# Performance work log

Measured on AMD Instinct MI355X. Metric: run time of the kernel, lower is better.

The kernel has to match this reference:

```python
import jax, jax.numpy as jnp
import numpy as np

B, T, Z, S, H = 32, 128, 100, 6, 64
F1, F2 = 512, 128


def setup_inputs() -> dict:
    key = jax.random.key(0)
    ks = jax.random.split(key, 11)
    g = lambda k, shape, sc: (jax.random.normal(k, shape, dtype=jnp.float32) * sc)
    return {
        "x": jax.random.normal(ks[0], (B, T, Z, S), dtype=jnp.float32),
        "W_ih": g(ks[1], (3 * H, S), 0.125),   # GRU input weights [r|z|n]
        "W_hh": g(ks[2], (3 * H, H), 0.125),   # GRU hidden weights [r|z|n]
        "b_ih": g(ks[3], (3 * H,), 0.125),
        "b_hh": g(ks[4], (3 * H,), 0.125),
        "w1": g(ks[5], (F1, H), 0.1),
        "b1": g(ks[6], (F1,), 0.1),
        "w2": g(ks[7], (F2, F1), 0.04),
        "b2": g(ks[8], (F2,), 0.04),
        "w3": g(ks[9], (1, F2), 0.09),
        "b3": g(ks[10], (1,), 0.09),
    }


def reference(x, W_ih, W_hh, b_ih, b_hh, w1, b1, w2, b2, w3, b3):
    b, t, z, s = x.shape
    h_dim = W_hh.shape[1]
    # Fuse the per-zone python loop into the batch dim, zone-major so the
    # final reshape matches torch.stack(a).view(-1, t, nzones).
    xm = jnp.transpose(x, (2, 0, 1, 3)).reshape(z * b, t, s)  # (ZB, T, S)
    # Precompute input projections for all timesteps (one big GEMM).
    gi_all = jnp.einsum('nts,gs->ntg', xm, W_ih) + b_ih        # (ZB, T, 3H)

    def step(h, gi):
        gh = h @ W_hh.T + b_hh
        r = jax.nn.sigmoid(gi[:, :h_dim] + gh[:, :h_dim])
        zg = jax.nn.sigmoid(gi[:, h_dim:2 * h_dim] + gh[:, h_dim:2 * h_dim])
        n = jnp.tanh(gi[:, 2 * h_dim:] + r * gh[:, 2 * h_dim:])
        h_new = (1.0 - zg) * n + zg * h
        return h_new, h_new

    h0 = jnp.zeros((z * b, h_dim), x.dtype)
    _, sx = jax.lax.scan(step, h0, jnp.swapaxes(gi_all, 0, 1))  # (T, ZB, H)
    sx = jnp.swapaxes(sx, 0, 1)                                  # (ZB, T, H)

    a1 = jax.nn.relu(sx @ w1.T + b1)
    a2 = jax.nn.relu(a1 @ w2.T + b2)
    a3 = a2 @ w3.T + b3                                          # (ZB, T, 1)
    return a3.reshape(-1, t, z)                                  # (B, T, Z)
```

## Files before the change

### kernel.cpp

```cpp
#include <hip/hip_runtime.h>
#include <stdint.h>

#define Tdim 128
#define Zdim 100
#define Sdim 6
#define Hdim 64
#define ZB   3200
#define F1   512
#define F2   128
#define Mrows (ZB * Tdim)

typedef _Float16 f16x8 __attribute__((ext_vector_type(8)));
typedef _Float16 f16x4 __attribute__((ext_vector_type(4)));
typedef float f32x4 __attribute__((ext_vector_type(4)));
typedef uint32_t u32x4 __attribute__((ext_vector_type(4)));

__device__ __forceinline__ float fast_rcp(float x) {
  return __builtin_amdgcn_rcpf(x);
}

__global__ __launch_bounds__(256) void prep_kernel(
    const float* __restrict__ W_ih, const float* __restrict__ W_hh,
    const float* __restrict__ w1, const float* __restrict__ w2,
    _Float16* __restrict__ Wf, _Float16* __restrict__ w1p,
    _Float16* __restrict__ w2p) {
  int i = blockIdx.x * 256 + threadIdx.x;
  if (i < 192 * 96) {
    int g = i / 96, k = i - g * 96;
    float v = (k < 64) ? W_hh[g * 64 + k] : ((k < 70) ? W_ih[g * 6 + (k - 64)] : 0.f);
    Wf[i] = (_Float16)v;
  }
  int j = i - 192 * 96;
  if (j >= 0 && j < 32768) {
    int kt = j >> 11, ntl = (j >> 10) & 1, kf = (j >> 9) & 1;
    int lane = (j >> 3) & 63, e = j & 7;
    int q = lane >> 4, c = lane & 15;
    int row = kt * 32 + ntl * 16 + c;
    int h = kf * 32 + q * 8 + e;
    w1p[j] = (_Float16)w1[row * 64 + h];
  }
  int l = j - 32768;
  if (l >= 0 && l < 65536) {
    int kt = l >> 12, nt = (l >> 9) & 7;
    int lane = (l >> 3) & 63, e = l & 7;
    int q = lane >> 4, c = lane & 15;
    int row = nt * 16 + c;
    int k = kt * 32 + q * 8 + e;
    w2p[l] = (_Float16)w2[row * 512 + k];
  }
}

__global__ __launch_bounds__(512, 1) void gru_kernel(
    const float* __restrict__ x, const _Float16* __restrict__ Wf,
    const float* __restrict__ b_ih, const float* __restrict__ b_hh,
    _Float16* __restrict__ sx) {
  __shared__ __align__(16) _Float16 hist[16][32][72];
  __shared__ __align__(16) _Float16 xs[Tdim][32][8];
  const int tid = threadIdx.x;
  const int lane = tid & 63;
  const int w8 = tid >> 6;
  const int s = w8 >> 2;
  const int w = w8 & 3;
  const int c = lane & 15;
  const int q = lane >> 4;
  const int s16c = s * 16 + c;

  for (int i = 0; i < 8; i++) {
    int idx = i * 512 + tid;
    int t = idx >> 5, row = idx & 31;
    int nr = blockIdx.x * 32 + row;
    const float* p = x + (size_t)(nr & 31) * (Tdim * Zdim * Sdim)
                       + (size_t)t * (Zdim * Sdim) + (size_t)(nr >> 5) * Sdim;
    f16x8 v;
    v[0] = (_Float16)p[0]; v[1] = (_Float16)p[1]; v[2] = (_Float16)p[2];
    v[3] = (_Float16)p[3]; v[4] = (_Float16)p[4]; v[5] = (_Float16)p[5];
    v[6] = (_Float16)0.f;  v[7] = (_Float16)0.f;
    *(f16x8*)&xs[t][row][0] = v;
  }

  const int gr0 = w * 16;
  const int gz0 = 64 + w * 16;
  const int gn0 = 128 + w * 16;

  f16x8 Ar[3], Az[3], Anh[2], Ani;
#pragma unroll
  for (int kf = 0; kf < 3; kf++) {
    Ar[kf] = *(const f16x8*)(Wf + (size_t)(gr0 + c) * 96 + kf * 32 + q * 8);
    Az[kf] = *(const f16x8*)(Wf + (size_t)(gz0 + c) * 96 + kf * 32 + q * 8);
  }
  Anh[0] = *(const f16x8*)(Wf + (size_t)(gn0 + c) * 96 + q * 8);
  Anh[1] = *(const f16x8*)(Wf + (size_t)(gn0 + c) * 96 + 32 + q * 8);
  Ani    = *(const f16x8*)(Wf + (size_t)(gn0 + c) * 96 + 64 + q * 8);

  f32x4 Cr, Cz, Cnh, Cni;
  {
    f32x4 bir = *(const f32x4*)(b_ih + gr0 + q * 4);
    f32x4 bhr = *(const f32x4*)(b_hh + gr0 + q * 4);
    f32x4 biz = *(const f32x4*)(b_ih + gz0 + q * 4);
    f32x4 bhz = *(const f32x4*)(b_hh + gz0 + q * 4);
#pragma unroll
    for (int r = 0; r < 4; r++) { Cr[r] = bir[r] + bhr[r]; Cz[r] = biz[r] + bhz[r]; }
    Cnh = *(const f32x4*)(b_hh + gn0 + q * 4);
    Cni = *(const f32x4*)(b_ih + gn0 + q * 4);
  }

  const uint32_t xmask = (q == 0) ? 0xffffffffu : 0u;

  __syncthreads();

  f16x8 Bh0 = {0, 0, 0, 0, 0, 0, 0, 0};
  f16x8 Bh1 = {0, 0, 0, 0, 0, 0, 0, 0};
  f32x4 hprev = {0.f, 0.f, 0.f, 0.f};

  f32x4 Dr_s, Dz_s, Dni_s;
  {
    u32x4 xv = *(const u32x4*)&xs[0][s16c][0];
    xv[0] &= xmask; xv[1] &= xmask; xv[2] &= xmask; xv[3] &= xmask;
    f16x8 Bx = *(f16x8*)&xv;
    Dni_s = __builtin_amdgcn_mfma_f32_16x16x32_f16(Ani, Bx, Cni, 0, 0, 0);
    Dr_s  = __builtin_amdgcn_mfma_f32_16x16x32_f16(Ar[2], Bx, Cr, 0, 0, 0);
    Dz_s  = __builtin_amdgcn_mfma_f32_16x16x32_f16(Az[2], Bx, Cz, 0, 0, 0);
  }

#pragma unroll 1
  for (int tch = 0; tch < 8; tch++) {
#pragma unroll 1
    for (int tc = 0; tc < 16; tc++) {
      const int t = tch * 16 + tc;
      f32x4 Dnh = __builtin_amdgcn_mfma_f32_16x16x32_f16(Anh[0], Bh0, Cnh, 0, 0, 0);
      f32x4 Dr  = __builtin_amdgcn_mfma_f32_16x16x32_f16(Ar[0], Bh0, Dr_s, 0, 0, 0);
      f32x4 Dz  = __builtin_amdgcn_mfma_f32_16x16x32_f16(Az[0], Bh0, Dz_s, 0, 0, 0);
      Dnh = __builtin_amdgcn_mfma_f32_16x16x32_f16(Anh[1], Bh1, Dnh, 0, 0, 0);
      Dr  = __builtin_amdgcn_mfma_f32_16x16x32_f16(Ar[1], Bh1, Dr, 0, 0, 0);
      Dz  = __builtin_amdgcn_mfma_f32_16x16x32_f16(Az[1], Bh1, Dz, 0, 0, 0);

      f16x4 pk;
#pragma unroll
      for (int r = 0; r < 4; r++) {
        float er = __expf(-Dr[r]);
        float rr = fast_rcp(1.f + er);
        float ez = __expf(-Dz[r]);
        float zg = fast_rcp(1.f + ez);
        float na = Dni_s[r] + rr * Dnh[r];
        float en = __expf(2.f * na);
        float nn = 1.f - 2.f * fast_rcp(en + 1.f);
        float hnew = nn + zg * (hprev[r] - nn);
        hprev[r] = hnew;
        pk[r] = (_Float16)hnew;
      }
      *(f16x4*)&hist[tc][s16c][w * 16 + q * 4] = pk;

      if (t + 1 < Tdim) {
        u32x4 xv = *(const u32x4*)&xs[t + 1][s16c][0];
        xv[0] &= xmask; xv[1] &= xmask; xv[2] &= xmask; xv[3] &= xmask;
        f16x8 Bx = *(f16x8*)&xv;
        Dni_s = __builtin_amdgcn_mfma_f32_16x16x32_f16(Ani, Bx, Cni, 0, 0, 0);
        Dr_s  = __builtin_amdgcn_mfma_f32_16x16x32_f16(Ar[2], Bx, Cr, 0, 0, 0);
        Dz_s  = __builtin_amdgcn_mfma_f32_16x16x32_f16(Az[2], Bx, Cz, 0, 0, 0);
      }
      __syncthreads();
      Bh0 = *(const f16x8*)&hist[tc][s16c][q * 8];
      Bh1 = *(const f16x8*)&hist[tc][s16c][32 + q * 8];
    }
    {
      const int t0 = tch * 16;
#pragma unroll
      for (int rr2 = 0; rr2 < 4; rr2++) {
        const int row = w8 * 4 + rr2;
        const int nrow = blockIdx.x * 32 + row;
        _Float16* dst = sx + (size_t)nrow * Tdim * Hdim + (size_t)t0 * Hdim;
#pragma unroll
        for (int it = 0; it < 2; it++) {
          int idx = it * 64 + lane;
          int tcc = idx >> 3, hd8 = idx & 7;
          f16x8 vv = *(const f16x8*)&hist[tcc][row][hd8 * 8];
          *(f16x8*)(dst + tcc * 64 + hd8 * 8) = vv;
        }
      }
      __syncthreads();
    }
  }
}

__global__ __launch_bounds__(256, 2) void mlp_kernel(
    const _Float16* __restrict__ sx, const _Float16* __restrict__ w1p,
    const _Float16* __restrict__ w2p, const float* __restrict__ b1,
    const float* __restrict__ b2, const float* __restrict__ w3,
    const float* __restrict__ b3, float* __restrict__ out) {
  __shared__ __align__(16) _Float16 w1s[32768];
  __shared__ __align__(16) _Float16 rep[4][4][512];
  const int tid = threadIdx.x;
  const int lane = tid & 63;
  const int wave = tid >> 6;
  const int c = lane & 15;
  const int q = lane >> 4;
  const size_t m0 = ((size_t)blockIdx.x * 4 + wave) * 64;

  {
    const u32x4* src = (const u32x4*)w1p;
    u32x4* dst = (u32x4*)w1s;
#pragma unroll
    for (int i = 0; i < 16; i++)
      dst[i * 256 + tid] = src[i * 256 + tid];
  }

  f16x8 Bs[4][2];
#pragma unroll
  for (int g = 0; g < 4; g++)
#pragma unroll
    for (int kk = 0; kk < 2; kk++)
      Bs[g][kk] = *(const f16x8*)(sx + (m0 + g * 16 + c) * Hdim + kk * 32 + q * 8);

  f32x4 acc2[4][8];
#pragma unroll
  for (int g = 0; g < 4; g++)
#pragma unroll
    for (int nt = 0; nt < 8; nt++) acc2[g][nt] = (f32x4){0.f, 0.f, 0.f, 0.f};

  __syncthreads();

  {
#pragma unroll
    for (int ntl = 0; ntl < 2; ntl++) {
      f16x8 A0 = *(const f16x8*)&w1s[ntl * 1024 + lane * 8];
      f16x8 A1 = *(const f16x8*)&w1s[ntl * 1024 + 512 + lane * 8];
      f32x4 bb = *(const f32x4*)(b1 + ntl * 16 + q * 4);
      const int roff = ((2 * ntl + (q >> 1)) * 16 + c) * 8 + (q & 1) * 4;
#pragma unroll
      for (int g = 0; g < 4; g++) {
        f32x4 cc = __builtin_amdgcn_mfma_f32_16x16x32_f16(A0, Bs[g][0], bb, 0, 0, 0);
        cc = __builtin_amdgcn_mfma_f32_16x16x32_f16(A1, Bs[g][1], cc, 0, 0, 0);
        f16x4 pk;
#pragma unroll
        for (int r = 0; r < 4; r++)
          pk[r] = (_Float16)(cc[r] > 0.f ? cc[r] : 0.f);
        *(f16x4*)&rep[wave][g][roff] = pk;
      }
    }
  }

#pragma unroll 1
  for (int kt = 0; kt < 16; kt++) {
    const int ktn = kt + 1;
    const bool more = (ktn < 16);
    f16x8 A2[8];
#pragma unroll
    for (int nt = 0; nt < 8; nt++)
      A2[nt] = *(const f16x8*)(w2p + (size_t)kt * 4096 + nt * 512 + lane * 8);
    f16x8 W0[2], W1[2];
    f32x4 bb[2];
    {
      const int kts = more ? ktn : kt;
#pragma unroll
      for (int ntl = 0; ntl < 2; ntl++) {
        W0[ntl] = *(const f16x8*)&w1s[kts * 2048 + ntl * 1024 + lane * 8];
        W1[ntl] = *(const f16x8*)&w1s[kts * 2048 + ntl * 1024 + 512 + lane * 8];
        bb[ntl] = *(const f32x4*)(b1 + kts * 32 + ntl * 16 + q * 4);
      }
    }
    f16x8 Ba[4];
#pragma unroll
    for (int g = 0; g < 4; g++)
      Ba[g] = *(const f16x8*)&rep[wave][g][lane * 8];

    if (more) {
#pragma unroll
      for (int ntl = 0; ntl < 2; ntl++) {
        const int roff = ((2 * ntl + (q >> 1)) * 16 + c) * 8 + (q & 1) * 4;
#pragma unroll
        for (int g = 0; g < 4; g++) {
          f32x4 cc = __builtin_amdgcn_mfma_f32_16x16x32_f16(W0[ntl], Bs[g][0], bb[ntl], 0, 0, 0);
          cc = __builtin_amdgcn_mfma_f32_16x16x32_f16(W1[ntl], Bs[g][1], cc, 0, 0, 0);
          f16x4 pk;
#pragma unroll
          for (int r = 0; r < 4; r++)
            pk[r] = (_Float16)(cc[r] > 0.f ? cc[r] : 0.f);
          *(f16x4*)&rep[wave][g][roff] = pk;
        }
      }
    }

#pragma unroll
    for (int nt = 0; nt < 8; nt++)
#pragma unroll
      for (int g = 0; g < 4; g++)
        acc2[g][nt] = __builtin_amdgcn_mfma_f32_16x16x32_f16(A2[nt], Ba[g], acc2[g][nt], 0, 0, 0);
  }

  float part[4] = {0.f, 0.f, 0.f, 0.f};
#pragma unroll
  for (int nt = 0; nt < 8; nt++) {
    f32x4 bb = *(const f32x4*)(b2 + nt * 16 + q * 4);
    f32x4 ww = *(const f32x4*)(w3 + nt * 16 + q * 4);
#pragma unroll
    for (int g = 0; g < 4; g++) {
#pragma unroll
      for (int r = 0; r < 4; r++) {
        float v = acc2[g][nt][r] + bb[r];
        v = v > 0.f ? v : 0.f;
        part[g] = fmaf(v, ww[r], part[g]);
      }
    }
  }
#pragma unroll
  for (int g = 0; g < 4; g++) {
    part[g] += __shfl_xor(part[g], 16, 64);
    part[g] += __shfl_xor(part[g], 32, 64);
  }
  float pv = (q == 0) ? part[0] : (q == 1) ? part[1] : (q == 2) ? part[2] : part[3];
  out[m0 + q * 16 + c] = pv + b3[0];
}

extern "C" void kernel_launch(void* const* d_in, const int* in_sizes, int n_in,
                              void* d_out, int out_size, void* d_ws, size_t ws_size,
                              hipStream_t stream) {
  const float* x    = (const float*)d_in[0];
  const float* W_ih = (const float*)d_in[1];
  const float* W_hh = (const float*)d_in[2];
  const float* b_ih = (const float*)d_in[3];
  const float* b_hh = (const float*)d_in[4];
  const float* w1   = (const float*)d_in[5];
  const float* b1   = (const float*)d_in[6];
  const float* w2   = (const float*)d_in[7];
  const float* b2   = (const float*)d_in[8];
  const float* w3   = (const float*)d_in[9];
  const float* b3   = (const float*)d_in[10];
  float* out = (float*)d_out;

  char* ws = (char*)d_ws;
  _Float16* sxf = (_Float16*)ws;
  _Float16* Wf  = (_Float16*)(ws + 52428800);
  _Float16* w1p = (_Float16*)(ws + 52428800 + 36864);
  _Float16* w2p = (_Float16*)(ws + 52428800 + 36864 + 65536);

  hipLaunchKernelGGL(prep_kernel, dim3(456), dim3(256), 0, stream,
                     W_ih, W_hh, w1, w2, Wf, w1p, w2p);
  hipLaunchKernelGGL(gru_kernel, dim3(ZB / 32), dim3(512), 0, stream,
                     x, Wf, b_ih, b_hh, sxf);
  hipLaunchKernelGGL(mlp_kernel, dim3(Mrows / 256), dim3(256), 0, stream,
                     sxf, w1p, w2p, b1, b2, w3, b3, out);
}
```

Baseline: 239.8 us.

## Fuse GRU and MLP into one producer-consumer kernel with chunk flags

```diff
diff --git a/kernel.cpp b/kernel.cpp
--- a/kernel.cpp
+++ b/kernel.cpp
@@ -9,6 +9,8 @@
 #define F1   512
 #define F2   128
 #define Mrows (ZB * Tdim)
+#define NGRU 100
+#define NMLP 800
 
 typedef _Float16 f16x8 __attribute__((ext_vector_type(8)));
 typedef _Float16 f16x4 __attribute__((ext_vector_type(4)));
@@ -23,8 +25,9 @@
     const float* __restrict__ W_ih, const float* __restrict__ W_hh,
     const float* __restrict__ w1, const float* __restrict__ w2,
     _Float16* __restrict__ Wf, _Float16* __restrict__ w1p,
-    _Float16* __restrict__ w2p) {
+    _Float16* __restrict__ w2p, unsigned int* __restrict__ sync) {
   int i = blockIdx.x * 256 + threadIdx.x;
+  if (i < 801) sync[i] = 0u;
   if (i < 192 * 96) {
     int g = i / 96, k = i - g * 96;
     float v = (k < 64) ? W_hh[g * 64 + k] : ((k < 70) ? W_ih[g * 6 + (k - 64)] : 0.f);
@@ -50,265 +53,288 @@
   }
 }
 
-__global__ __launch_bounds__(512, 1) void gru_kernel(
+__global__ __launch_bounds__(512, 2) void fused_kernel(
     const float* __restrict__ x, const _Float16* __restrict__ Wf,
     const float* __restrict__ b_ih, const float* __restrict__ b_hh,
-    _Float16* __restrict__ sx) {
-  __shared__ __align__(16) _Float16 hist[16][32][72];
-  __shared__ __align__(16) _Float16 xs[Tdim][32][8];
+    _Float16* __restrict__ sx, const _Float16* __restrict__ w1p,
+    const _Float16* __restrict__ w2p, const float* __restrict__ b1,
+    const float* __restrict__ b2, const float* __restrict__ w3,
+    const float* __restrict__ b3, float* __restrict__ out,
+    unsigned int* __restrict__ flags, unsigned int* __restrict__ ticket) {
+  union SmemU {
+    struct { _Float16 hist[16][32][72]; _Float16 xs[Tdim][32][8]; } g;
+    struct { _Float16 w1s[32768]; _Float16 rep[8][4][512]; } m;
+  };
+  __shared__ __align__(16) SmemU smem;
+  __shared__ int s_tk;
   const int tid = threadIdx.x;
+  if (tid == 0) s_tk = (int)atomicAdd(ticket, 1u);
+  __syncthreads();
+  const int tk = s_tk;
+
   const int lane = tid & 63;
   const int w8 = tid >> 6;
-  const int s = w8 >> 2;
-  const int w = w8 & 3;
   const int c = lane & 15;
   const int q = lane >> 4;
-  const int s16c = s * 16 + c;
-
-  for (int i = 0; i < 8; i++) {
-    int idx = i * 512 + tid;
-    int t = idx >> 5, row = idx & 31;
-    int nr = blockIdx.x * 32 + row;
-    const float* p = x + (size_t)(nr & 31) * (Tdim * Zdim * Sdim)
-                       + (size_t)t * (Zdim * Sdim) + (size_t)(nr >> 5) * Sdim;
-    f16x8 v;
-    v[0] = (_Float16)p[0]; v[1] = (_Float16)p[1]; v[2] = (_Float16)p[2];
-    v[3] = (_Float16)p[3]; v[4] = (_Float16)p[4]; v[5] = (_Float16)p[5];
-    v[6] = (_Float16)0.f;  v[7] = (_Float16)0.f;
-    *(f16x8*)&xs[t][row][0] = v;
-  }
-
-  const int gr0 = w * 16;
-  const int gz0 = 64 + w * 16;
-  const int gn0 = 128 + w * 16;
-
-  f16x8 Ar[3], Az[3], Anh[2], Ani;
-#pragma unroll
-  for (int kf = 0; kf < 3; kf++) {
-    Ar[kf] = *(const f16x8*)(Wf + (size_t)(gr0 + c) * 96 + kf * 32 + q * 8);
-    Az[kf] = *(const f16x8*)(Wf + (size_t)(gz0 + c) * 96 + kf * 32 + q * 8);
-  }
-  Anh[0] = *(const f16x8*)(Wf + (size_t)(gn0 + c) * 96 + q * 8);
-  Anh[1] = *(const f16x8*)(Wf + (size_t)(gn0 + c) * 96 + 32 + q * 8);
-  Ani    = *(const f16x8*)(Wf + (size_t)(gn0 + c) * 96 + 64 + q * 8);
-
-  f32x4 Cr, Cz, Cnh, Cni;
-  {
-    f32x4 bir = *(const f32x4*)(b_ih + gr0 + q * 4);
-    f32x4 bhr = *(const f32x4*)(b_hh + gr0 + q * 4);
-    f32x4 biz = *(const f32x4*)(b_ih + gz0 + q * 4);
-    f32x4 bhz = *(const f32x4*)(b_hh + gz0 + q * 4);
-#pragma unroll
-    for (int r = 0; r < 4; r++) { Cr[r] = bir[r] + bhr[r]; Cz[r] = biz[r] + bhz[r]; }
-    Cnh = *(const f32x4*)(b_hh + gn0 + q * 4);
-    Cni = *(const f32x4*)(b_ih + gn0 + q * 4);
-  }
-
-  const uint32_t xmask = (q == 0) ? 0xffffffffu : 0u;
-
-  __syncthreads();
-
-  f16x8 Bh0 = {0, 0, 0, 0, 0, 0, 0, 0};
-  f16x8 Bh1 = {0, 0, 0, 0, 0, 0, 0, 0};
-  f32x4 hprev = {0.f, 0.f, 0.f, 0.f};
-
-  f32x4 Dr_s, Dz_s, Dni_s;
-  {
-    u32x4 xv = *(const u32x4*)&xs[0][s16c][0];
-    xv[0] &= xmask; xv[1] &= xmask; xv[2] &= xmask; xv[3] &= xmask;
-    f16x8 Bx = *(f16x8*)&xv;
-    Dni_s = __builtin_amdgcn_mfma_f32_16x16x32_f16(Ani, Bx, Cni, 0, 0, 0);
-    Dr_s  = __builtin_amdgcn_mfma_f32_16x16x32_f16(Ar[2], Bx, Cr, 0, 0, 0);
-    Dz_s  = __builtin_amdgcn_mfma_f32_16x16x32_f16(Az[2], Bx, Cz, 0, 0, 0);
-  }
+
+  if (tk < NGRU) {
+    const int gb = tk;
+    auto& hist = smem.g.hist;
+    auto& xs = smem.g.xs;
+    const int s = w8 >> 2;
+    const int w = w8 & 3;
+    const int s16c = s * 16 + c;
+
+    for (int i = 0; i < 8; i++) {
+      int idx = i * 512 + tid;
+      int t = idx >> 5, row = idx & 31;
+      int nr = gb * 32 + row;
+      const float* p = x + (size_t)(nr & 31) * (Tdim * Zdim * Sdim)
+                         + (size_t)t * (Zdim * Sdim) + (size_t)(nr >> 5) * Sdim;
+      f16x8 v;
+      v[0] = (_Float16)p[0]; v[1] = (_Float16)p[1]; v[2] = (_Float16)p[2];
+      v[3] = (_Float16)p[3]; v[4] = (_Float16)p[4]; v[5] = (_Float16)p[5];
+      v[6] = (_Float16)0.f;  v[7] = (_Float16)0.f;
+      *(f16x8*)&xs[t][row][0] = v;
+    }
+
+    const int gr0 = w * 16;
+    const int gz0 = 64 + w * 16;
+    const int gn0 = 128 + w * 16;
+
+    f16x8 Ar[3], Az[3], Anh[2], Ani;
+#pragma unroll
+    for (int kf = 0; kf < 3; kf++) {
+      Ar[kf] = *(const f16x8*)(Wf + (size_t)(gr0 + c) * 96 + kf * 32 + q * 8);
+      Az[kf] = *(const f16x8*)(Wf + (size_t)(gz0 + c) * 96 + kf * 32 + q * 8);
+    }
+    Anh[0] = *(const f16x8*)(Wf + (size_t)(gn0 + c) * 96 + q * 8);
+    Anh[1] = *(const f16x8*)(Wf + (size_t)(gn0 + c) * 96 + 32 + q * 8);
+    Ani    = *(const f16x8*)(Wf + (size_t)(gn0 + c) * 96 + 64 + q * 8);
+
+    f32x4 Cr, Cz, Cnh, Cni;
+    {
+      f32x4 bir = *(const f32x4*)(b_ih + gr0 + q * 4);
+      f32x4 bhr = *(const f32x4*)(b_hh + gr0 + q * 4);
+      f32x4 biz = *(const f32x4*)(b_ih + gz0 + q * 4);
+      f32x4 bhz = *(const f32x4*)(b_hh + gz0 + q * 4);
+#pragma unroll
+      for (int r = 0; r < 4; r++) { Cr[r] = bir[r] + bhr[r]; Cz[r] = biz[r] + bhz[r]; }
+      Cnh = *(const f32x4*)(b_hh + gn0 + q * 4);
+      Cni = *(const f32x4*)(b_ih + gn0 + q * 4);
+    }
+
+    const uint32_t xmask = (q == 0) ? 0xffffffffu : 0u;
+
+    __syncthreads();
+
+    f16x8 Bh0 = {0, 0, 0, 0, 0, 0, 0, 0};
+    f16x8 Bh1 = {0, 0, 0, 0, 0, 0, 0, 0};
+    f32x4 hprev = {0.f, 0.f, 0.f, 0.f};
+
+    f32x4 Dr_s, Dz_s, Dni_s;
+    {
+      u32x4 xv = *(const u32x4*)&xs[0][s16c][0];
+      xv[0] &= xmask; xv[1] &= xmask; xv[2] &= xmask; xv[3] &= xmask;
+      f16x8 Bx = *(f16x8*)&xv;
+      Dni_s = __builtin_amdgcn_mfma_f32_16x16x32_f16(Ani, Bx, Cni, 0, 0, 0);
+      Dr_s  = __builtin_amdgcn_mfma_f32_16x16x32_f16(Ar[2], Bx, Cr, 0, 0, 0);
+      Dz_s  = __builtin_amdgcn_mfma_f32_16x16x32_f16(Az[2], Bx, Cz, 0, 0, 0);
+    }
 
 #pragma unroll 1
-  for (int tch = 0; tch < 8; tch++) {
+    for (int tch = 0; tch < 8; tch++) {
 #pragma unroll 1
-    for (int tc = 0; tc < 16; tc++) {
-      const int t = tch * 16 + tc;
-      f32x4 Dnh = __builtin_amdgcn_mfma_f32_16x16x32_f16(Anh[0], Bh0, Cnh, 0, 0, 0);
-      f32x4 Dr  = __builtin_amdgcn_mfma_f32_16x16x32_f16(Ar[0], Bh0, Dr_s, 0, 0, 0);
-      f32x4 Dz  = __builtin_amdgcn_mfma_f32_16x16x32_f16(Az[0], Bh0, Dz_s, 0, 0, 0);
-      Dnh = __builtin_amdgcn_mfma_f32_16x16x32_f16(Anh[1], Bh1, Dnh, 0, 0, 0);
-      Dr  = __builtin_amdgcn_mfma_f32_16x16x32_f16(Ar[1], Bh1, Dr, 0, 0, 0);
-      Dz  = __builtin_amdgcn_mfma_f32_16x16x32_f16(Az[1], Bh1, Dz, 0, 0, 0);
-
-      f16x4 pk;
-#pragma unroll
-      for (int r = 0; r < 4; r++) {
-        float er = __expf(-Dr[r]);
-        float rr = fast_rcp(1.f + er);
-        float ez = __expf(-Dz[r]);
-        float zg = fast_rcp(1.f + ez);
-        float na = Dni_s[r] + rr * Dnh[r];
-        float en = __expf(2.f * na);
-        float nn = 1.f - 2.f * fast_rcp(en + 1.f);
-        float hnew = nn + zg * (hprev[r] - nn);
-        hprev[r] = hnew;
-        pk[r] = (_Float16)hnew;
-      }
-      *(f16x4*)&hist[tc][s16c][w * 16 + q * 4] = pk;
-
-      if (t + 1 < Tdim) {
-        u32x4 xv = *(const u32x4*)&xs[t + 1][s16c][0];
-        xv[0] &= xmask; xv[1] &= xmask; xv[2] &= xmask; xv[3] &= xmask;
-        f16x8 Bx = *(f16x8*)&xv;
-        Dni_s = __builtin_amdgcn_mfma_f32_16x16x32_f16(Ani, Bx, Cni, 0, 0, 0);
-        Dr_s  = __builtin_amdgcn_mfma_f32_16x16x32_f16(Ar[2], Bx, Cr, 0, 0, 0);
-        Dz_s  = __builtin_amdgcn_mfma_f32_16x16x32_f16(Az[2], Bx, Cz, 0, 0, 0);
-      }
-      __syncthreads();
-      Bh0 = *(const f16x8*)&hist[tc][s16c][q * 8];
-      Bh1 = *(const f16x8*)&hist[tc][s16c][32 + q * 8];
-    }
+      for (int tc = 0; tc < 16; tc++) {
+        const int t = tch * 16 + tc;
+        f32x4 Dnh = __builtin_amdgcn_mfma_f32_16x16x32_f16(Anh[0], Bh0, Cnh, 0, 0, 0);
+        f32x4 Dr  = __builtin_amdgcn_mfma_f32_16x16x32_f16(Ar[0], Bh0, Dr_s, 0, 0, 0);
+        f32x4 Dz  = __builtin_amdgcn_mfma_f32_16x16x32_f16(Az[0], Bh0, Dz_s, 0, 0, 0);
+        Dnh = __builtin_amdgcn_mfma_f32_16x16x32_f16(Anh[1], Bh1, Dnh, 0, 0, 0);
+        Dr  = __builtin_amdgcn_mfma_f32_16x16x32_f16(Ar[1], Bh1, Dr, 0, 0, 0);
+        Dz  = __builtin_amdgcn_mfma_f32_16x16x32_f16(Az[1], Bh1, Dz, 0, 0, 0);
+
+        f16x4 pk;
+#pragma unroll
+        for (int r = 0; r < 4; r++) {
+          float er = __expf(-Dr[r]);
+          float rr = fast_rcp(1.f + er);
+          float ez = __expf(-Dz[r]);
+          float zg = fast_rcp(1.f + ez);
+          float na = Dni_s[r] + rr * Dnh[r];
+          float en = __expf(2.f * na);
+          float nn = 1.f - 2.f * fast_rcp(en + 1.f);
+          float hnew = nn + zg * (hprev[r] - nn);
+          hprev[r] = hnew;
+          pk[r] = (_Float16)hnew;
+        }
+        *(f16x4*)&hist[tc][s16c][w * 16 + q * 4] = pk;
+
+        if (t + 1 < Tdim) {
+          u32x4 xv = *(const u32x4*)&xs[t + 1][s16c][0];
+          xv[0] &= xmask; xv[1] &= xmask; xv[2] &= xmask; xv[3] &= xmask;
+          f16x8 Bx = *(f16x8*)&xv;
+          Dni_s = __builtin_amdgcn_mfma_f32_16x16x32_f16(Ani, Bx, Cni, 0, 0, 0);
+          Dr_s  = __builtin_amdgcn_mfma_f32_16x16x32_f16(Ar[2], Bx, Cr, 0, 0, 0);
+          Dz_s  = __builtin_amdgcn_mfma_f32_16x16x32_f16(Az[2], Bx, Cz, 0, 0, 0);
+        }
+        __syncthreads();
+        Bh0 = *(const f16x8*)&hist[tc][s16c][q * 8];
+        Bh1 = *(const f16x8*)&hist[tc][s16c][32 + q * 8];
+      }
+      {
+        const int t0 = tch * 16;
+#pragma unroll
+        for (int rr2 = 0; rr2 < 4; rr2++) {
+          const int row = w8 * 4 + rr2;
+          const int nrow = gb * 32 + row;
+          _Float16* dst = sx + (size_t)nrow * Tdim * Hdim + (size_t)t0 * Hdim;
+#pragma unroll
+          for (int it = 0; it < 2; it++) {
+            int idx = it * 64 + lane;
+            int tcc = idx >> 3, hd8 = idx & 7;
+            f16x8 vv = *(const f16x8*)&hist[tcc][row][hd8 * 8];
+            *(f16x8*)(dst + tcc * 64 + hd8 * 8) = vv;
+          }
+        }
+        __syncthreads();
+        if (tid == 0) {
+          __threadfence();
+          atomicAdd(&flags[gb * 8 + tch], 1u);
+        }
+      }
+    }
+  } else {
+    const int mid = tk - NGRU;
+    const int gbm = mid % NGRU;
+    const int ch  = mid / NGRU;
+    auto& w1s = smem.m.w1s;
+    auto& rep = smem.m.rep;
+
     {
-      const int t0 = tch * 16;
-#pragma unroll
-      for (int rr2 = 0; rr2 < 4; rr2++) {
-        const int row = w8 * 4 + rr2;
-        const int nrow = blockIdx.x * 32 + row;
-        _Float16* dst = sx + (size_t)nrow * Tdim * Hdim + (size_t)t0 * Hdim;
-#pragma unroll
-        for (int it = 0; it < 2; it++) {
-          int idx = it * 64 + lane;
-          int tcc = idx >> 3, hd8 = idx & 7;
-          f16x8 vv = *(const f16x8*)&hist[tcc][row][hd8 * 8];
-          *(f16x8*)(dst + tcc * 64 + hd8 * 8) = vv;
-        }
-      }
-      __syncthreads();
-    }
-  }
-}
-
-__global__ __launch_bounds__(256, 2) void mlp_kernel(
-    const _Float16* __restrict__ sx, const _Float16* __restrict__ w1p,
-    const _Float16* __restrict__ w2p, const float* __restrict__ b1,
-    const float* __restrict__ b2, const float* __restrict__ w3,
-    const float* __restrict__ b3, float* __restrict__ out) {
-  __shared__ __align__(16) _Float16 w1s[32768];
-  __shared__ __align__(16) _Float16 rep[4][4][512];
-  const int tid = threadIdx.x;
-  const int lane = tid & 63;
-  const int wave = tid >> 6;
-  const int c = lane & 15;
-  const int q = lane >> 4;
-  const size_t m0 = ((size_t)blockIdx.x * 4 + wave) * 64;
-
-  {
-    const u32x4* src = (const u32x4*)w1p;
-    u32x4* dst = (u32x4*)w1s;
-#pragma unroll
-    for (int i = 0; i < 16; i++)
-      dst[i * 256 + tid] = src[i * 256 + tid];
-  }
-
-  f16x8 Bs[4][2];
-#pragma unroll
-  for (int g = 0; g < 4; g++)
-#pragma unroll
-    for (int kk = 0; kk < 2; kk++)
-      Bs[g][kk] = *(const f16x8*)(sx + (m0 + g * 16 + c) * Hdim + kk * 32 + q * 8);
-
-  f32x4 acc2[4][8];
-#pragma unroll
-  for (int g = 0; g < 4; g++)
-#pragma unroll
-    for (int nt = 0; nt < 8; nt++) acc2[g][nt] = (f32x4){0.f, 0.f, 0.f, 0.f};
-
-  __syncthreads();
-
-  {
-#pragma unroll
-    for (int ntl = 0; ntl < 2; ntl++) {
-      f16x8 A0 = *(const f16x8*)&w1s[ntl * 1024 + lane * 8];
-      f16x8 A1 = *(const f16x8*)&w1s[ntl * 1024 + 512 + lane * 8];
-      f32x4 bb = *(const f32x4*)(b1 + ntl * 16 + q * 4);
-      const int roff = ((2 * ntl + (q >> 1)) * 16 + c) * 8 + (q & 1) * 4;
-#pragma unroll
-      for (int g = 0; g < 4; g++) {
-        f32x4 cc = __builtin_amdgcn_mfma_f32_16x16x32_f16(A0, Bs[g][0], bb, 0, 0, 0);
-        cc = __builtin_amdgcn_mfma_f32_16x16x32_f16(A1, Bs[g][1], cc, 0, 0, 0);
-        f16x4 pk;
-#pragma unroll
-        for (int r = 0; r < 4; r++)
-          pk[r] = (_Float16)(cc[r] > 0.f ? cc[r] : 0.f);
-        *(f16x4*)&rep[wave][g][roff] = pk;
-      }
-    }
-  }
-
-#pragma unroll 1
-  for (int kt = 0; kt < 16; kt++) {
-    const int ktn = kt + 1;
-    const bool more = (ktn < 16);
-    f16x8 A2[8];
-#pragma unroll
-    for (int nt = 0; nt < 8; nt++)
-      A2[nt] = *(const f16x8*)(w2p + (size_t)kt * 4096 + nt * 512 + lane * 8);
-    f16x8 W0[2], W1[2];
-    f32x4 bb[2];
+      const u32x4* srcw = (const u32x4*)w1p;
+      u32x4* dstw = (u32x4*)w1s;
+#pragma unroll
+      for (int i = 0; i < 8; i++)
+        dstw[i * 512 + tid] = srcw[i * 512 + tid];
+    }
+    if (tid == 0) {
+      while (__hip_atomic_load(&flags[gbm * 8 + ch], __ATOMIC_RELAXED,
+                               __HIP_MEMORY_SCOPE_AGENT) == 0u)
+        __builtin_amdgcn_s_sleep(2);
+      (void)__hip_atomic_load(&flags[gbm * 8 + ch], __ATOMIC_ACQUIRE,
+                              __HIP_MEMORY_SCOPE_AGENT);
+    }
+    __syncthreads();
+
+    const int seqB = gbm * 32 + w8 * 4;
+    const size_t tB = (size_t)ch * 16;
+
+    f16x8 Bs[4][2];
+#pragma unroll
+    for (int g = 0; g < 4; g++)
+#pragma unroll
+      for (int kk = 0; kk < 2; kk++)
+        Bs[g][kk] = *(const f16x8*)(sx + ((size_t)(seqB + g) * Tdim + tB + c) * Hdim
+                                    + kk * 32 + q * 8);
+
+    f32x4 acc2[4][8];
+#pragma unroll
+    for (int g = 0; g < 4; g++)
+#pragma unroll
+      for (int nt = 0; nt < 8; nt++) acc2[g][nt] = (f32x4){0.f, 0.f, 0.f, 0.f};
+
     {
-      const int kts = more ? ktn : kt;
 #pragma unroll
       for (int ntl = 0; ntl < 2; ntl++) {
-        W0[ntl] = *(const f16x8*)&w1s[kts * 2048 + ntl * 1024 + lane * 8];
-        W1[ntl] = *(const f16x8*)&w1s[kts * 2048 + ntl * 1024 + 512 + lane * 8];
-        bb[ntl] = *(const f32x4*)(b1 + kts * 32 + ntl * 16 + q * 4);
-      }
-    }
-    f16x8 Ba[4];
-#pragma unroll
-    for (int g = 0; g < 4; g++)
-      Ba[g] = *(const f16x8*)&rep[wave][g][lane * 8];
-
-    if (more) {
-#pragma unroll
-      for (int ntl = 0; ntl < 2; ntl++) {
+        f16x8 A0 = *(const f16x8*)&w1s[ntl * 1024 + lane * 8];
+        f16x8 A1 = *(const f16x8*)&w1s[ntl * 1024 + 512 + lane * 8];
+        f32x4 bb = *(const f32x4*)(b1 + ntl * 16 + q * 4);
         const int roff = ((2 * ntl + (q >> 1)) * 16 + c) * 8 + (q & 1) * 4;
 #pragma unroll
         for (int g = 0; g < 4; g++) {
-          f32x4 cc = __builtin_amdgcn_mfma_f32_16x16x32_f16(W0[ntl], Bs[g][0], bb[ntl], 0, 0, 0);
-          cc = __builtin_amdgcn_mfma_f32_16x16x32_f16(W1[ntl], Bs[g][1], cc, 0, 0, 0);
+          f32x4 cc = __builtin_amdgcn_mfma_f32_16x16x32_f16(A0, Bs[g][0], bb, 0, 0, 0);
+          cc = __builtin_amdgcn_mfma_f32_16x16x32_f16(A1, Bs[g][1], cc, 0, 0, 0);
           f16x4 pk;
 #pragma unroll
           for (int r = 0; r < 4; r++)
             pk[r] = (_Float16)(cc[r] > 0.f ? cc[r] : 0.f);
-          *(f16x4*)&rep[wave][g][roff] = pk;
-        }
-      }
-    }
-
-#pragma unroll
-    for (int nt = 0; nt < 8; nt++)
+          *(f16x4*)&rep[w8][g][roff] = pk;
+        }
+      }
+    }
+
+#pragma unroll 1
+    for (int kt = 0; kt < 16; kt++) {
+      const int ktn = kt + 1;
+      const bool more = (ktn < 16);
+      f16x8 A2[8];
+#pragma unroll
+      for (int nt = 0; nt < 8; nt++)
+        A2[nt] = *(const f16x8*)(w2p + (size_t)kt * 4096 + nt * 512 + lane * 8);
+      f16x8 W0[2], W1[2];
+      f32x4 bb[2];
+      {
+        const int kts = more ? ktn : kt;
+#pragma unroll
+        for (int ntl = 0; ntl < 2; ntl++) {
+          W0[ntl] = *(const f16x8*)&w1s[kts * 2048 + ntl * 1024 + lane * 8];
+          W1[ntl] = *(const f16x8*)&w1s[kts * 2048 + ntl * 1024 + 512 + lane * 8];
+          bb[ntl] = *(const f32x4*)(b1 + kts * 32 + ntl * 16 + q * 4);
+        }
+      }
+      f16x8 Ba[4];
 #pragma unroll
       for (int g = 0; g < 4; g++)
-        acc2[g][nt] = __builtin_amdgcn_mfma_f32_16x16x32_f16(A2[nt], Ba[g], acc2[g][nt], 0, 0, 0);
+        Ba[g] = *(const f16x8*)&rep[w8][g][lane * 8];
+
+      if (more) {
+#pragma unroll
+        for (int ntl = 0; ntl < 2; ntl++) {
+          const int roff = ((2 * ntl + (q >> 1)) * 16 + c) * 8 + (q & 1) * 4;
+#pragma unroll
+          for (int g = 0; g < 4; g++) {
+            f32x4 cc = __builtin_amdgcn_mfma_f32_16x16x32_f16(W0[ntl], Bs[g][0], bb[ntl], 0, 0, 0);
+            cc = __builtin_amdgcn_mfma_f32_16x16x32_f16(W1[ntl], Bs[g][1], cc, 0, 0, 0);
+            f16x4 pk;
+#pragma unroll
+            for (int r = 0; r < 4; r++)
+              pk[r] = (_Float16)(cc[r] > 0.f ? cc[r] : 0.f);
+            *(f16x4*)&rep[w8][g][roff] = pk;
+          }
+        }
+      }
+
+#pragma unroll
+      for (int nt = 0; nt < 8; nt++)
+#pragma unroll
+        for (int g = 0; g < 4; g++)
+          acc2[g][nt] = __builtin_amdgcn_mfma_f32_16x16x32_f16(A2[nt], Ba[g], acc2[g][nt], 0, 0, 0);
+    }
+
+    float part[4] = {0.f, 0.f, 0.f, 0.f};
+#pragma unroll
+    for (int nt = 0; nt < 8; nt++) {
+      f32x4 bb = *(const f32x4*)(b2 + nt * 16 + q * 4);
+      f32x4 ww = *(const f32x4*)(w3 + nt * 16 + q * 4);
+#pragma unroll
+      for (int g = 0; g < 4; g++) {
+#pragma unroll
+        for (int r = 0; r < 4; r++) {
+          float v = acc2[g][nt][r] + bb[r];
+          v = v > 0.f ? v : 0.f;
+          part[g] = fmaf(v, ww[r], part[g]);
+        }
+      }
+    }
+#pragma unroll
+    for (int g = 0; g < 4; g++) {
+      part[g] += __shfl_xor(part[g], 16, 64);
+      part[g] += __shfl_xor(part[g], 32, 64);
+    }
+    float pv = (q == 0) ? part[0] : (q == 1) ? part[1] : (q == 2) ? part[2] : part[3];
+    out[(size_t)(seqB + q) * Tdim + tB + c] = pv + b3[0];
   }
-
-  float part[4] = {0.f, 0.f, 0.f, 0.f};
-#pragma unroll
-  for (int nt = 0; nt < 8; nt++) {
-    f32x4 bb = *(const f32x4*)(b2 + nt * 16 + q * 4);
-    f32x4 ww = *(const f32x4*)(w3 + nt * 16 + q * 4);
-#pragma unroll
-    for (int g = 0; g < 4; g++) {
-#pragma unroll
-      for (int r = 0; r < 4; r++) {
-        float v = acc2[g][nt][r] + bb[r];
-        v = v > 0.f ? v : 0.f;
-        part[g] = fmaf(v, ww[r], part[g]);
-      }
-    }
-  }
-#pragma unroll
-  for (int g = 0; g < 4; g++) {
-    part[g] += __shfl_xor(part[g], 16, 64);
-    part[g] += __shfl_xor(part[g], 32, 64);
-  }
-  float pv = (q == 0) ? part[0] : (q == 1) ? part[1] : (q == 2) ? part[2] : part[3];
-  out[m0 + q * 16 + c] = pv + b3[0];
 }
 
 extern "C" void kernel_launch(void* const* d_in, const int* in_sizes, int n_in,
@@ -332,11 +358,13 @@
   _Float16* Wf  = (_Float16*)(ws + 52428800);
   _Float16* w1p = (_Float16*)(ws + 52428800 + 36864);
   _Float16* w2p = (_Float16*)(ws + 52428800 + 36864 + 65536);
+  unsigned int* syncb = (unsigned int*)(ws + 52428800 + 36864 + 65536 + 131072);
+  unsigned int* flags  = syncb;
+  unsigned int* ticket = syncb + 800;
 
   hipLaunchKernelGGL(prep_kernel, dim3(456), dim3(256), 0, stream,
-                     W_ih, W_hh, w1, w2, Wf, w1p, w2p);
-  hipLaunchKernelGGL(gru_kernel, dim3(ZB / 32), dim3(512), 0, stream,
-                     x, Wf, b_ih, b_hh, sxf);
-  hipLaunchKernelGGL(mlp_kernel, dim3(Mrows / 256), dim3(256), 0, stream,
-                     sxf, w1p, w2p, b1, b2, w3, b3, out);
+                     W_ih, W_hh, w1, w2, Wf, w1p, w2p, syncb);
+  hipLaunchKernelGGL(fused_kernel, dim3(NGRU + NMLP), dim3(512), 0, stream,
+                     x, Wf, b_ih, b_hh, sxf, w1p, w2p, b1, b2, w3, b3, out,
+                     flags, ticket);
 }
```

Result: faster. 229.3 us (-4.4%).

## Run GRU recurrence in a single wave per 16 sequences, removing block barriers

Applied to the files above, without the earlier changes.

```diff
diff --git a/kernel.cpp b/kernel.cpp
--- a/kernel.cpp
+++ b/kernel.cpp
@@ -13,6 +13,7 @@
 typedef _Float16 f16x8 __attribute__((ext_vector_type(8)));
 typedef _Float16 f16x4 __attribute__((ext_vector_type(4)));
 typedef float f32x4 __attribute__((ext_vector_type(4)));
+typedef float f32x2 __attribute__((ext_vector_type(2)));
 typedef uint32_t u32x4 __attribute__((ext_vector_type(4)));
 
 __device__ __forceinline__ float fast_rcp(float x) {
@@ -50,134 +51,155 @@
   }
 }
 
-__global__ __launch_bounds__(512, 1) void gru_kernel(
+__global__ __launch_bounds__(64, 1) void gru_kernel(
     const float* __restrict__ x, const _Float16* __restrict__ Wf,
     const float* __restrict__ b_ih, const float* __restrict__ b_hh,
     _Float16* __restrict__ sx) {
-  __shared__ __align__(16) _Float16 hist[16][32][72];
-  __shared__ __align__(16) _Float16 xs[Tdim][32][8];
-  const int tid = threadIdx.x;
-  const int lane = tid & 63;
-  const int w8 = tid >> 6;
-  const int s = w8 >> 2;
-  const int w = w8 & 3;
+  __shared__ __align__(16) _Float16 hist[16][16][72];
+  const int lane = threadIdx.x & 63;
   const int c = lane & 15;
   const int q = lane >> 4;
-  const int s16c = s * 16 + c;
-
-  for (int i = 0; i < 8; i++) {
-    int idx = i * 512 + tid;
-    int t = idx >> 5, row = idx & 31;
-    int nr = blockIdx.x * 32 + row;
-    const float* p = x + (size_t)(nr & 31) * (Tdim * Zdim * Sdim)
-                       + (size_t)t * (Zdim * Sdim) + (size_t)(nr >> 5) * Sdim;
-    f16x8 v;
-    v[0] = (_Float16)p[0]; v[1] = (_Float16)p[1]; v[2] = (_Float16)p[2];
-    v[3] = (_Float16)p[3]; v[4] = (_Float16)p[4]; v[5] = (_Float16)p[5];
-    v[6] = (_Float16)0.f;  v[7] = (_Float16)0.f;
-    *(f16x8*)&xs[t][row][0] = v;
-  }
-
-  const int gr0 = w * 16;
-  const int gz0 = 64 + w * 16;
-  const int gn0 = 128 + w * 16;
-
-  f16x8 Ar[3], Az[3], Anh[2], Ani;
-#pragma unroll
-  for (int kf = 0; kf < 3; kf++) {
-    Ar[kf] = *(const f16x8*)(Wf + (size_t)(gr0 + c) * 96 + kf * 32 + q * 8);
-    Az[kf] = *(const f16x8*)(Wf + (size_t)(gz0 + c) * 96 + kf * 32 + q * 8);
-  }
-  Anh[0] = *(const f16x8*)(Wf + (size_t)(gn0 + c) * 96 + q * 8);
-  Anh[1] = *(const f16x8*)(Wf + (size_t)(gn0 + c) * 96 + 32 + q * 8);
-  Ani    = *(const f16x8*)(Wf + (size_t)(gn0 + c) * 96 + 64 + q * 8);
-
-  f32x4 Cr, Cz, Cnh, Cni;
-  {
-    f32x4 bir = *(const f32x4*)(b_ih + gr0 + q * 4);
-    f32x4 bhr = *(const f32x4*)(b_hh + gr0 + q * 4);
-    f32x4 biz = *(const f32x4*)(b_ih + gz0 + q * 4);
-    f32x4 bhz = *(const f32x4*)(b_hh + gz0 + q * 4);
-#pragma unroll
-    for (int r = 0; r < 4; r++) { Cr[r] = bir[r] + bhr[r]; Cz[r] = biz[r] + bhz[r]; }
-    Cnh = *(const f32x4*)(b_hh + gn0 + q * 4);
-    Cni = *(const f32x4*)(b_ih + gn0 + q * 4);
+  const int wid = blockIdx.x;
+
+  const int nr = wid * 16 + c;
+  const float* px = x + (size_t)(nr & 31) * (Tdim * Zdim * Sdim)
+                      + (size_t)(nr >> 5) * Sdim;
+
+  f16x8 A[3][4][3];
+#pragma unroll
+  for (int g = 0; g < 3; g++)
+#pragma unroll
+    for (int nt = 0; nt < 4; nt++)
+#pragma unroll
+      for (int kf = 0; kf < 3; kf++)
+        A[g][nt][kf] = *(const f16x8*)(Wf + (size_t)(g * 64 + nt * 16 + c) * 96
+                                       + kf * 32 + q * 8);
+
+  f32x4 Crz[2][4], Cnh[4], Cni[4];
+#pragma unroll
+  for (int g = 0; g < 2; g++)
+#pragma unroll
+    for (int nt = 0; nt < 4; nt++) {
+      f32x4 bi = *(const f32x4*)(b_ih + g * 64 + nt * 16 + q * 4);
+      f32x4 bh = *(const f32x4*)(b_hh + g * 64 + nt * 16 + q * 4);
+#pragma unroll
+      for (int r = 0; r < 4; r++) Crz[g][nt][r] = bi[r] + bh[r];
+    }
+#pragma unroll
+  for (int nt = 0; nt < 4; nt++) {
+    Cnh[nt] = *(const f32x4*)(b_hh + 128 + nt * 16 + q * 4);
+    Cni[nt] = *(const f32x4*)(b_ih + 128 + nt * 16 + q * 4);
   }
 
   const uint32_t xmask = (q == 0) ? 0xffffffffu : 0u;
-
-  __syncthreads();
 
   f16x8 Bh0 = {0, 0, 0, 0, 0, 0, 0, 0};
   f16x8 Bh1 = {0, 0, 0, 0, 0, 0, 0, 0};
-  f32x4 hprev = {0.f, 0.f, 0.f, 0.f};
-
-  f32x4 Dr_s, Dz_s, Dni_s;
+  f32x4 hprev[4] = {{0.f, 0.f, 0.f, 0.f}, {0.f, 0.f, 0.f, 0.f},
+                    {0.f, 0.f, 0.f, 0.f}, {0.f, 0.f, 0.f, 0.f}};
+
+  f32x4 Sr[4], Sz[4], Sni[4];
+  f32x2 xa, xb, xc;
+  xa = *(const f32x2*)(px + 0);
+  xb = *(const f32x2*)(px + 2);
+  xc = *(const f32x2*)(px + 4);
+  f16x8 Bx;
   {
-    u32x4 xv = *(const u32x4*)&xs[0][s16c][0];
+    Bx[0] = (_Float16)xa[0]; Bx[1] = (_Float16)xa[1];
+    Bx[2] = (_Float16)xb[0]; Bx[3] = (_Float16)xb[1];
+    Bx[4] = (_Float16)xc[0]; Bx[5] = (_Float16)xc[1];
+    Bx[6] = (_Float16)0.f;   Bx[7] = (_Float16)0.f;
+    u32x4 xv = *(u32x4*)&Bx;
     xv[0] &= xmask; xv[1] &= xmask; xv[2] &= xmask; xv[3] &= xmask;
-    f16x8 Bx = *(f16x8*)&xv;
-    Dni_s = __builtin_amdgcn_mfma_f32_16x16x32_f16(Ani, Bx, Cni, 0, 0, 0);
-    Dr_s  = __builtin_amdgcn_mfma_f32_16x16x32_f16(Ar[2], Bx, Cr, 0, 0, 0);
-    Dz_s  = __builtin_amdgcn_mfma_f32_16x16x32_f16(Az[2], Bx, Cz, 0, 0, 0);
+    Bx = *(f16x8*)&xv;
+  }
+#pragma unroll
+  for (int nt = 0; nt < 4; nt++) {
+    Sr[nt]  = __builtin_amdgcn_mfma_f32_16x16x32_f16(A[0][nt][2], Bx, Crz[0][nt], 0, 0, 0);
+    Sz[nt]  = __builtin_amdgcn_mfma_f32_16x16x32_f16(A[1][nt][2], Bx, Crz[1][nt], 0, 0, 0);
+    Sni[nt] = __builtin_amdgcn_mfma_f32_16x16x32_f16(A[2][nt][2], Bx, Cni[nt], 0, 0, 0);
   }
 
 #pragma unroll 1
-  for (int tch = 0; tch < 8; tch++) {
-#pragma unroll 1
-    for (int tc = 0; tc < 16; tc++) {
-      const int t = tch * 16 + tc;
-      f32x4 Dnh = __builtin_amdgcn_mfma_f32_16x16x32_f16(Anh[0], Bh0, Cnh, 0, 0, 0);
-      f32x4 Dr  = __builtin_amdgcn_mfma_f32_16x16x32_f16(Ar[0], Bh0, Dr_s, 0, 0, 0);
-      f32x4 Dz  = __builtin_amdgcn_mfma_f32_16x16x32_f16(Az[0], Bh0, Dz_s, 0, 0, 0);
-      Dnh = __builtin_amdgcn_mfma_f32_16x16x32_f16(Anh[1], Bh1, Dnh, 0, 0, 0);
-      Dr  = __builtin_amdgcn_mfma_f32_16x16x32_f16(Ar[1], Bh1, Dr, 0, 0, 0);
-      Dz  = __builtin_amdgcn_mfma_f32_16x16x32_f16(Az[1], Bh1, Dz, 0, 0, 0);
-
+  for (int t = 0; t < Tdim; t++) {
+    const int tn = (t + 1 < Tdim) ? t + 1 : Tdim - 1;
+    const float* pn = px + (size_t)tn * (Zdim * Sdim);
+    xa = *(const f32x2*)(pn + 0);
+    xb = *(const f32x2*)(pn + 2);
+    xc = *(const f32x2*)(pn + 4);
+
+    f32x4 Dr[4], Dz[4], Dnh[4];
+#pragma unroll
+    for (int nt = 0; nt < 4; nt++)
+      Dnh[nt] = __builtin_amdgcn_mfma_f32_16x16x32_f16(A[2][nt][0], Bh0, Cnh[nt], 0, 0, 0);
+#pragma unroll
+    for (int nt = 0; nt < 4; nt++)
+      Dr[nt] = __builtin_amdgcn_mfma_f32_16x16x32_f16(A[0][nt][0], Bh0, Sr[nt], 0, 0, 0);
+#pragma unroll
+    for (int nt = 0; nt < 4; nt++)
+      Dz[nt] = __builtin_amdgcn_mfma_f32_16x16x32_f16(A[1][nt][0], Bh0, Sz[nt], 0, 0, 0);
+#pragma unroll
+    for (int nt = 0; nt < 4; nt++)
+      Dnh[nt] = __builtin_amdgcn_mfma_f32_16x16x32_f16(A[2][nt][1], Bh1, Dnh[nt], 0, 0, 0);
+#pragma unroll
+    for (int nt = 0; nt < 4; nt++)
+      Dr[nt] = __builtin_amdgcn_mfma_f32_16x16x32_f16(A[0][nt][1], Bh1, Dr[nt], 0, 0, 0);
+#pragma unroll
+    for (int nt = 0; nt < 4; nt++)
+      Dz[nt] = __builtin_amdgcn_mfma_f32_16x16x32_f16(A[1][nt][1], Bh1, Dz[nt], 0, 0, 0);
+
+    const int tc = t & 15;
+#pragma unroll
+    for (int nt = 0; nt < 4; nt++) {
       f16x4 pk;
 #pragma unroll
       for (int r = 0; r < 4; r++) {
-        float er = __expf(-Dr[r]);
+        float er = __expf(-Dr[nt][r]);
         float rr = fast_rcp(1.f + er);
-        float ez = __expf(-Dz[r]);
+        float ez = __expf(-Dz[nt][r]);
         float zg = fast_rcp(1.f + ez);
-        float na = Dni_s[r] + rr * Dnh[r];
+        float na = Sni[nt][r] + rr * Dnh[nt][r];
         float en = __expf(2.f * na);
         float nn = 1.f - 2.f * fast_rcp(en + 1.f);
-        float hnew = nn + zg * (hprev[r] - nn);
-        hprev[r] = hnew;
+        float hnew = nn + zg * (hprev[nt][r] - nn);
+        hprev[nt][r] = hnew;
         pk[r] = (_Float16)hnew;
       }
-      *(f16x4*)&hist[tc][s16c][w * 16 + q * 4] = pk;
-
-      if (t + 1 < Tdim) {
-        u32x4 xv = *(const u32x4*)&xs[t + 1][s16c][0];
-        xv[0] &= xmask; xv[1] &= xmask; xv[2] &= xmask; xv[3] &= xmask;
-        f16x8 Bx = *(f16x8*)&xv;
-        Dni_s = __builtin_amdgcn_mfma_f32_16x16x32_f16(Ani, Bx, Cni, 0, 0, 0);
-        Dr_s  = __builtin_amdgcn_mfma_f32_16x16x32_f16(Ar[2], Bx, Cr, 0, 0, 0);
-        Dz_s  = __builtin_amdgcn_mfma_f32_16x16x32_f16(Az[2], Bx, Cz, 0, 0, 0);
-      }
-      __syncthreads();
-      Bh0 = *(const f16x8*)&hist[tc][s16c][q * 8];
-      Bh1 = *(const f16x8*)&hist[tc][s16c][32 + q * 8];
-    }
+      *(f16x4*)&hist[tc][c][nt * 16 + q * 4] = pk;
+    }
+
     {
-      const int t0 = tch * 16;
-#pragma unroll
-      for (int rr2 = 0; rr2 < 4; rr2++) {
-        const int row = w8 * 4 + rr2;
-        const int nrow = blockIdx.x * 32 + row;
-        _Float16* dst = sx + (size_t)nrow * Tdim * Hdim + (size_t)t0 * Hdim;
-#pragma unroll
-        for (int it = 0; it < 2; it++) {
+      Bx[0] = (_Float16)xa[0]; Bx[1] = (_Float16)xa[1];
+      Bx[2] = (_Float16)xb[0]; Bx[3] = (_Float16)xb[1];
+      Bx[4] = (_Float16)xc[0]; Bx[5] = (_Float16)xc[1];
+      Bx[6] = (_Float16)0.f;   Bx[7] = (_Float16)0.f;
+      u32x4 xv = *(u32x4*)&Bx;
+      xv[0] &= xmask; xv[1] &= xmask; xv[2] &= xmask; xv[3] &= xmask;
+      Bx = *(f16x8*)&xv;
+    }
+#pragma unroll
+    for (int nt = 0; nt < 4; nt++) {
+      Sr[nt]  = __builtin_amdgcn_mfma_f32_16x16x32_f16(A[0][nt][2], Bx, Crz[0][nt], 0, 0, 0);
+      Sz[nt]  = __builtin_amdgcn_mfma_f32_16x16x32_f16(A[1][nt][2], Bx, Crz[1][nt], 0, 0, 0);
+      Sni[nt] = __builtin_amdgcn_mfma_f32_16x16x32_f16(A[2][nt][2], Bx, Cni[nt], 0, 0, 0);
+    }
+
+    Bh0 = *(const f16x8*)&hist[tc][c][q * 8];
+    Bh1 = *(const f16x8*)&hist[tc][c][32 + q * 8];
+
+    if (tc == 15) {
+      const int t0 = t - 15;
+#pragma unroll 1
+      for (int row = 0; row < 16; ++row) {
+        _Float16* dst = sx + ((size_t)(wid * 16 + row) * Tdim + t0) * Hdim;
+#pragma unroll
+        for (int it = 0; it < 2; ++it) {
           int idx = it * 64 + lane;
           int tcc = idx >> 3, hd8 = idx & 7;
           f16x8 vv = *(const f16x8*)&hist[tcc][row][hd8 * 8];
-          *(f16x8*)(dst + tcc * 64 + hd8 * 8) = vv;
+          *(f16x8*)(dst + (size_t)tcc * 64 + hd8 * 8) = vv;
         }
       }
-      __syncthreads();
     }
   }
 }
@@ -335,7 +357,7 @@
 
   hipLaunchKernelGGL(prep_kernel, dim3(456), dim3(256), 0, stream,
                      W_ih, W_hh, w1, w2, Wf, w1p, w2p);
-  hipLaunchKernelGGL(gru_kernel, dim3(ZB / 32), dim3(512), 0, stream,
+  hipLaunchKernelGGL(gru_kernel, dim3(ZB / 16), dim3(64), 0, stream,
                      x, Wf, b_ih, b_hh, sxf);
   hipLaunchKernelGGL(mlp_kernel, dim3(Mrows / 256), dim3(256), 0, stream,
                      sxf, w1p, w2p, b1, b2, w3, b3, out);
```

After: 292.5 us. +22.0%, slower.
